# Kernel optimization log

Hardware: AMD Instinct MI355X
Metric: run time of the kernel (lower is better)

## Reference

```python
import jax, jax.numpy as jnp
import numpy as np

LUT_DIM = 33  # standard 33^3 color LUT


def setup_inputs() -> dict:
    key = jax.random.key(0)
    k1, k2 = jax.random.split(key)
    # learned 3D LUT: [out_channels=3, D_b, D_g, D_r]
    lut = jax.random.normal(k1, (3, LUT_DIM, LUT_DIM, LUT_DIM), dtype=jnp.float32) * 0.1
    # input image batch in [0, 1): [B, 3, H, W]
    x = jax.random.uniform(k2, (4, 3, 1024, 1024), dtype=jnp.float32)
    return {"lut": lut, "x": x}


def reference(lut, x):
    """Trilinear interpolation of a 3D color LUT (image-adaptive-3DLUT forward).

    lut: [3, D, D, D] laid out as lut[c, ib, ig, ir] (flat index ir + ig*D + ib*D*D)
    x:   [B, 3, H, W] with channels (r, g, b) in [0, 1]
    returns: [B, 3, H, W]
    """
    dim = lut.shape[-1]
    scale = dim - 1  # 1 / binsize

    r, g, b = x[:, 0], x[:, 1], x[:, 2]  # each [B, H, W]

    def cell(c):
        s = c * scale
        idx = jnp.clip(jnp.floor(s), 0, scale - 1).astype(jnp.int32)
        return idx, s - idx.astype(s.dtype)  # integer cell, fractional offset

    ir, dr = cell(r)
    ig, dg = cell(g)
    ib, db = cell(b)

    lut_flat = lut.reshape(3, -1)  # [3, D^3], tiny and cache-resident

    out = jnp.zeros((3,) + r.shape, dtype=x.dtype)  # [3, B, H, W]
    # 8 corners of the enclosing LUT cell, trilinear weights
    for or_ in (0, 1):
        wr = dr if or_ else (1.0 - dr)
        for og in (0, 1):
            wg = dg if og else (1.0 - dg)
            for ob in (0, 1):
                wb = db if ob else (1.0 - db)
                flat = ((ib + ob) * dim + (ig + og)) * dim + (ir + or_)  # [B, H, W]
                corner = lut_flat[:, flat]  # gather -> [3, B, H, W]
                out = out + (wr * wg * wb)[None] * corner

    return jnp.transpose(out, (1, 0, 2, 3))  # [B, 3, H, W]
```

## Files before the change

### kernel.cpp

```cpp
#include <hip/hip_runtime.h>
#include <hip/hip_fp16.h>


#define LUT_D     33
#define LUT_DD    (LUT_D * LUT_D)
#define LUT_N     (LUT_D * LUT_D * LUT_D)
#define CH_STRIDE 35940
#define STAGE_G   (CH_STRIDE / 4)
#define HW4       (1024 * 1024 / 4)
#define NGROUPS   (4 * HW4)
#define NCHUNKS   256
#define THREADS   1024
#define ITERS     (NGROUPS / NCHUNKS / THREADS)

typedef float vfloat4 __attribute__((ext_vector_type(4)));

__device__ __forceinline__ unsigned int pack2(float a, float b) {
    union { __half2 h; unsigned int u; } cv;
    cv.h = __floats2half2_rn(a, b);
    return cv.u;
}
__device__ __forceinline__ float2 unpack2(unsigned int p) {
    union { unsigned int u; __half2 h; } cv;
    cv.u = p;
    return __half22float2(cv.h);
}

__global__ __launch_bounds__(256)
void lut_pack_kernel(const float* __restrict__ lut, unsigned int* __restrict__ W) {
    const int t = blockIdx.x * 256 + (int)threadIdx.x;
    if (t >= 3 * LUT_N) return;
    const int c = t / LUT_N;
    const int i = t - c * LUT_N;
    const float a = lut[t];
    const float b = (i + 1 < LUT_N) ? lut[t + 1] : 0.0f;
    W[c * CH_STRIDE + i] = pack2(a, b);
}

__global__ __launch_bounds__(THREADS)
void lut3d_trilerp_kernel(const unsigned int* __restrict__ W,
                          const float* __restrict__ x,
                          float* __restrict__ out) {
    extern __shared__ __align__(16) unsigned int P[];

    const int bx   = blockIdx.x;
    const int xcd  = bx & 7;
    const int c    = (bx >> 3) % 3;
    const int chunk = (bx / 24) * 8 + xcd;

    const unsigned int* src = W + c * CH_STRIDE;
    for (int s = 0; s < 9; ++s) {
        const int gid = s * THREADS + (int)threadIdx.x;
        if (gid < STAGE_G) {
            __builtin_amdgcn_global_load_lds(
                (const __attribute__((address_space(1))) void*)(src + gid * 4),
                (__attribute__((address_space(3))) void*)(P + gid * 4),
                16, 0, 0);
        }
    }
    __syncthreads();

    const float4* x4 = (const float4*)x;
    float4*       o4 = (float4*)out;

    const int g0 = chunk * (NGROUPS / NCHUNKS) + (int)threadIdx.x;

    float4 R[ITERS], G[ITERS], B[ITERS];
    int obase[ITERS];
#pragma unroll
    for (int it = 0; it < ITERS; ++it) {
        const int g     = g0 + it * THREADS;
        const int b_img = g >> 18;
        const int hw4   = g & (HW4 - 1);
        const int ibase = b_img * 3 * HW4 + hw4;
        R[it] = x4[ibase];
        G[it] = x4[ibase + HW4];
        B[it] = x4[ibase + 2 * HW4];
        obase[it] = ibase + c * HW4;
    }

#pragma unroll
    for (int it = 0; it < ITERS; ++it) {
        const float rr[4] = {R[it].x, R[it].y, R[it].z, R[it].w};
        const float gg[4] = {G[it].x, G[it].y, G[it].z, G[it].w};
        const float bb[4] = {B[it].x, B[it].y, B[it].z, B[it].w};

        int   idx[4];
        float dr[4], dg[4], db[4];
#pragma unroll
        for (int k = 0; k < 4; ++k) {
            const float sr = rr[k] * 32.0f;
            const float sg = gg[k] * 32.0f;
            const float sb = bb[k] * 32.0f;
            const float fr = fminf(fmaxf(floorf(sr), 0.0f), 31.0f);
            const float fg = fminf(fmaxf(floorf(sg), 0.0f), 31.0f);
            const float fb = fminf(fmaxf(floorf(sb), 0.0f), 31.0f);
            dr[k] = sr - fr;
            dg[k] = sg - fg;
            db[k] = sb - fb;
            idx[k] = ((int)fb * LUT_D + (int)fg) * LUT_D + (int)fr;
        }

        unsigned int q00[4], q01[4], q10[4], q11[4];
#pragma unroll
        for (int k = 0; k < 4; ++k) {
            q00[k] = P[idx[k]];
            q01[k] = P[idx[k] + LUT_D];
            q10[k] = P[idx[k] + LUT_DD];
            q11[k] = P[idx[k] + LUT_DD + LUT_D];
        }

        float oo[4];
#pragma unroll
        for (int k = 0; k < 4; ++k) {
            const float2 a00 = unpack2(q00[k]);
            const float2 a01 = unpack2(q01[k]);
            const float2 a10 = unpack2(q10[k]);
            const float2 a11 = unpack2(q11[k]);
            const float l00 = a00.x + dr[k] * (a00.y - a00.x);
            const float l01 = a01.x + dr[k] * (a01.y - a01.x);
            const float l10 = a10.x + dr[k] * (a10.y - a10.x);
            const float l11 = a11.x + dr[k] * (a11.y - a11.x);
            const float l0  = l00 + dg[k] * (l01 - l00);
            const float l1  = l10 + dg[k] * (l11 - l10);
            oo[k] = l0 + db[k] * (l1 - l0);
        }

        vfloat4 v = {oo[0], oo[1], oo[2], oo[3]};
        __builtin_nontemporal_store(v, (vfloat4*)&o4[obase[it]]);
    }
}

extern "C" void kernel_launch(void* const* d_in, const int* in_sizes, int n_in,
                              void* d_out, int out_size, void* d_ws, size_t ws_size,
                              hipStream_t stream) {
    const float*  lut = (const float*)d_in[0];
    const float*  x   = (const float*)d_in[1];
    float*        out = (float*)d_out;
    unsigned int* W   = (unsigned int*)d_ws;

    const int pack_grid = (3 * LUT_N + 255) / 256;
    lut_pack_kernel<<<pack_grid, 256, 0, stream>>>(lut, W);

    const int grid = 3 * NCHUNKS;
    const size_t lds_bytes = (size_t)STAGE_G * 16;
    lut3d_trilerp_kernel<<<grid, THREADS, lds_bytes, stream>>>(W, x, out);
}
```

Baseline: 118.0 us.

## Store LUT as plain fp16 in LDS, halving footprint, and double grid chunks

Replaces the paired half2 LUT layout (each entry plus its r-neighbour) with a plain fp16 array, halving LDS per block to about 72KB. Each pixel now does 8 scalar half LDS reads instead of 4 packed 32-bit reads. Chunk count doubles to 512, input loads are interleaved with compute instead of prefetched, and the launch bound requests higher occupancy. The aim is more resident blocks per CU to hide latency, at the cost of twice as many LDS gather instructions and more staging overhead from the larger grid.

```diff
diff --git a/kernel.cpp b/kernel.cpp
--- a/kernel.cpp
+++ b/kernel.cpp
@@ -2,59 +2,47 @@
 #include <hip/hip_fp16.h>
 
 
-#define LUT_D     33
-#define LUT_DD    (LUT_D * LUT_D)
-#define LUT_N     (LUT_D * LUT_D * LUT_D)
-#define CH_STRIDE 35940
-#define STAGE_G   (CH_STRIDE / 4)
-#define HW4       (1024 * 1024 / 4)
-#define NGROUPS   (4 * HW4)
-#define NCHUNKS   256
-#define THREADS   1024
-#define ITERS     (NGROUPS / NCHUNKS / THREADS)
+#define LUT_D    33
+#define LUT_DD   (LUT_D * LUT_D)
+#define LUT_N    (LUT_D * LUT_D * LUT_D)
+#define CH_H     36000
+#define STAGE_G4 4500
+#define HW4      (1024 * 1024 / 4)
+#define NG       (4 * HW4)
+#define NCHUNKS  512
+#define THREADS  1024
+#define GPB      (NG / NCHUNKS)
+#define ITERS    (GPB / THREADS)
 
 typedef float vfloat4 __attribute__((ext_vector_type(4)));
 
-__device__ __forceinline__ unsigned int pack2(float a, float b) {
-    union { __half2 h; unsigned int u; } cv;
-    cv.h = __floats2half2_rn(a, b);
-    return cv.u;
-}
-__device__ __forceinline__ float2 unpack2(unsigned int p) {
-    union { unsigned int u; __half2 h; } cv;
-    cv.u = p;
-    return __half22float2(cv.h);
-}
-
 __global__ __launch_bounds__(256)
-void lut_pack_kernel(const float* __restrict__ lut, unsigned int* __restrict__ W) {
+void lut_pack_kernel(const float* __restrict__ lut, __half* __restrict__ W) {
     const int t = blockIdx.x * 256 + (int)threadIdx.x;
     if (t >= 3 * LUT_N) return;
     const int c = t / LUT_N;
     const int i = t - c * LUT_N;
-    const float a = lut[t];
-    const float b = (i + 1 < LUT_N) ? lut[t + 1] : 0.0f;
-    W[c * CH_STRIDE + i] = pack2(a, b);
+    W[c * CH_H + i] = __float2half(lut[t]);
 }
 
-__global__ __launch_bounds__(THREADS)
-void lut3d_trilerp_kernel(const unsigned int* __restrict__ W,
+__global__ __launch_bounds__(THREADS, 8)
+void lut3d_trilerp_kernel(const __half* __restrict__ W,
                           const float* __restrict__ x,
                           float* __restrict__ out) {
-    extern __shared__ __align__(16) unsigned int P[];
+    extern __shared__ __align__(16) __half sl[];
 
-    const int bx   = blockIdx.x;
-    const int xcd  = bx & 7;
-    const int c    = (bx >> 3) % 3;
+    const int bx    = blockIdx.x;
+    const int xcd   = bx & 7;
+    const int c     = (bx >> 3) % 3;
     const int chunk = (bx / 24) * 8 + xcd;
 
-    const unsigned int* src = W + c * CH_STRIDE;
-    for (int s = 0; s < 9; ++s) {
+    const char* srcb = (const char*)W + (size_t)c * (CH_H * 2);
+    for (int s = 0; s < 5; ++s) {
         const int gid = s * THREADS + (int)threadIdx.x;
-        if (gid < STAGE_G) {
+        if (gid < STAGE_G4) {
             __builtin_amdgcn_global_load_lds(
-                (const __attribute__((address_space(1))) void*)(src + gid * 4),
-                (__attribute__((address_space(3))) void*)(P + gid * 4),
+                (const __attribute__((address_space(1))) void*)(srcb + gid * 16),
+                (__attribute__((address_space(3))) void*)((char*)sl + gid * 16),
                 16, 0, 0);
         }
     }
@@ -63,35 +51,30 @@
     const float4* x4 = (const float4*)x;
     float4*       o4 = (float4*)out;
 
-    const int g0 = chunk * (NGROUPS / NCHUNKS) + (int)threadIdx.x;
+    const int g0 = chunk * GPB + (int)threadIdx.x;
 
-    float4 R[ITERS], G[ITERS], B[ITERS];
-    int obase[ITERS];
 #pragma unroll
     for (int it = 0; it < ITERS; ++it) {
         const int g     = g0 + it * THREADS;
         const int b_img = g >> 18;
         const int hw4   = g & (HW4 - 1);
         const int ibase = b_img * 3 * HW4 + hw4;
-        R[it] = x4[ibase];
-        G[it] = x4[ibase + HW4];
-        B[it] = x4[ibase + 2 * HW4];
-        obase[it] = ibase + c * HW4;
-    }
 
-#pragma unroll
-    for (int it = 0; it < ITERS; ++it) {
-        const float rr[4] = {R[it].x, R[it].y, R[it].z, R[it].w};
-        const float gg[4] = {G[it].x, G[it].y, G[it].z, G[it].w};
-        const float bb[4] = {B[it].x, B[it].y, B[it].z, B[it].w};
+        const float4 r4 = x4[ibase];
+        const float4 g4 = x4[ibase + HW4];
+        const float4 b4 = x4[ibase + 2 * HW4];
+
+        const float RR[4] = {r4.x, r4.y, r4.z, r4.w};
+        const float GG[4] = {g4.x, g4.y, g4.z, g4.w};
+        const float BB[4] = {b4.x, b4.y, b4.z, b4.w};
 
         int   idx[4];
         float dr[4], dg[4], db[4];
 #pragma unroll
         for (int k = 0; k < 4; ++k) {
-            const float sr = rr[k] * 32.0f;
-            const float sg = gg[k] * 32.0f;
-            const float sb = bb[k] * 32.0f;
+            const float sr = RR[k] * 32.0f;
+            const float sg = GG[k] * 32.0f;
+            const float sb = BB[k] * 32.0f;
             const float fr = fminf(fmaxf(floorf(sr), 0.0f), 31.0f);
             const float fg = fminf(fmaxf(floorf(sg), 0.0f), 31.0f);
             const float fb = fminf(fmaxf(floorf(sb), 0.0f), 31.0f);
@@ -101,48 +84,60 @@
             idx[k] = ((int)fb * LUT_D + (int)fg) * LUT_D + (int)fr;
         }
 
-        unsigned int q00[4], q01[4], q10[4], q11[4];
-#pragma unroll
-        for (int k = 0; k < 4; ++k) {
-            q00[k] = P[idx[k]];
-            q01[k] = P[idx[k] + LUT_D];
-            q10[k] = P[idx[k] + LUT_DD];
-            q11[k] = P[idx[k] + LUT_DD + LUT_D];
-        }
-
         float oo[4];
 #pragma unroll
-        for (int k = 0; k < 4; ++k) {
-            const float2 a00 = unpack2(q00[k]);
-            const float2 a01 = unpack2(q01[k]);
-            const float2 a10 = unpack2(q10[k]);
-            const float2 a11 = unpack2(q11[k]);
-            const float l00 = a00.x + dr[k] * (a00.y - a00.x);
-            const float l01 = a01.x + dr[k] * (a01.y - a01.x);
-            const float l10 = a10.x + dr[k] * (a10.y - a10.x);
-            const float l11 = a11.x + dr[k] * (a11.y - a11.x);
-            const float l0  = l00 + dg[k] * (l01 - l00);
-            const float l1  = l10 + dg[k] * (l11 - l10);
-            oo[k] = l0 + db[k] * (l1 - l0);
+        for (int kk = 0; kk < 4; kk += 2) {
+            __half h[2][8];
+#pragma unroll
+            for (int j = 0; j < 2; ++j) {
+                const int i0 = idx[kk + j];
+                h[j][0] = sl[i0];
+                h[j][1] = sl[i0 + 1];
+                h[j][2] = sl[i0 + LUT_D];
+                h[j][3] = sl[i0 + LUT_D + 1];
+                h[j][4] = sl[i0 + LUT_DD];
+                h[j][5] = sl[i0 + LUT_DD + 1];
+                h[j][6] = sl[i0 + LUT_DD + LUT_D];
+                h[j][7] = sl[i0 + LUT_DD + LUT_D + 1];
+            }
+#pragma unroll
+            for (int j = 0; j < 2; ++j) {
+                const int k = kk + j;
+                const float v000 = __half2float(h[j][0]);
+                const float v001 = __half2float(h[j][1]);
+                const float v010 = __half2float(h[j][2]);
+                const float v011 = __half2float(h[j][3]);
+                const float v100 = __half2float(h[j][4]);
+                const float v101 = __half2float(h[j][5]);
+                const float v110 = __half2float(h[j][6]);
+                const float v111 = __half2float(h[j][7]);
+                const float l00 = v000 + dr[k] * (v001 - v000);
+                const float l01 = v010 + dr[k] * (v011 - v010);
+                const float l10 = v100 + dr[k] * (v101 - v100);
+                const float l11 = v110 + dr[k] * (v111 - v110);
+                const float l0  = l00 + dg[k] * (l01 - l00);
+                const float l1  = l10 + dg[k] * (l11 - l10);
+                oo[k] = l0 + db[k] * (l1 - l0);
+            }
         }
 
         vfloat4 v = {oo[0], oo[1], oo[2], oo[3]};
-        __builtin_nontemporal_store(v, (vfloat4*)&o4[obase[it]]);
+        __builtin_nontemporal_store(v, (vfloat4*)&o4[ibase + c * HW4]);
     }
 }
 
 extern "C" void kernel_launch(void* const* d_in, const int* in_sizes, int n_in,
                               void* d_out, int out_size, void* d_ws, size_t ws_size,
                               hipStream_t stream) {
-    const float*  lut = (const float*)d_in[0];
-    const float*  x   = (const float*)d_in[1];
-    float*        out = (float*)d_out;
-    unsigned int* W   = (unsigned int*)d_ws;
+    const float* lut = (const float*)d_in[0];
+    const float* x   = (const float*)d_in[1];
+    float*       out = (float*)d_out;
+    __half*      W   = (__half*)d_ws;
 
     const int pack_grid = (3 * LUT_N + 255) / 256;
     lut_pack_kernel<<<pack_grid, 256, 0, stream>>>(lut, W);
 
     const int grid = 3 * NCHUNKS;
-    const size_t lds_bytes = (size_t)STAGE_G * 16;
+    const size_t lds_bytes = (size_t)CH_H * 2;
     lut3d_trilerp_kernel<<<grid, THREADS, lds_bytes, stream>>>(W, x, out);
 }
```

Result: slower. 171.9 us (+45.7%).

## Software-pipeline pixel loads and LDS gathers with double buffering

Applied to the files above, without the earlier changes.

Replaces the load-everything-then-compute loop with a two-stage software pipeline. Input loads run two iterations ahead and index computation plus LDS gathers run one iteration ahead of the interpolation math and store. The first input loads are now issued before the LUT-staging barrier, so they overlap with the LDS fill. This targets exposed global-memory and LDS latency and lowers register pressure from holding all iterations' inputs at once, but the fully unrolled macro code may still leave the compiler's schedule largely unchanged.

```diff
diff --git a/kernel.cpp b/kernel.cpp
--- a/kernel.cpp
+++ b/kernel.cpp
@@ -8,10 +8,10 @@
 #define CH_STRIDE 35940
 #define STAGE_G   (CH_STRIDE / 4)
 #define HW4       (1024 * 1024 / 4)
-#define NGROUPS   (4 * HW4)
+#define NG        (4 * HW4)
 #define NCHUNKS   256
 #define THREADS   1024
-#define ITERS     (NGROUPS / NCHUNKS / THREADS)
+#define ITERS     (NG / NCHUNKS / THREADS)
 
 typedef float vfloat4 __attribute__((ext_vector_type(4)));
 
@@ -20,7 +20,7 @@
     cv.h = __floats2half2_rn(a, b);
     return cv.u;
 }
-__device__ __forceinline__ float2 unpack2(unsigned int p) {
+__device__ __forceinline__ float2 up2(unsigned int p) {
     union { unsigned int u; __half2 h; } cv;
     cv.u = p;
     return __half22float2(cv.h);
@@ -43,9 +43,9 @@
                           float* __restrict__ out) {
     extern __shared__ __align__(16) unsigned int P[];
 
-    const int bx   = blockIdx.x;
-    const int xcd  = bx & 7;
-    const int c    = (bx >> 3) % 3;
+    const int bx    = blockIdx.x;
+    const int xcd   = bx & 7;
+    const int c     = (bx >> 3) % 3;
     const int chunk = (bx / 24) * 8 + xcd;
 
     const unsigned int* src = W + c * CH_STRIDE;
@@ -58,77 +58,108 @@
                 16, 0, 0);
         }
     }
-    __syncthreads();
 
     const float4* x4 = (const float4*)x;
     float4*       o4 = (float4*)out;
+    const int g0 = chunk * (NG / NCHUNKS) + (int)threadIdx.x;
 
-    const int g0 = chunk * (NGROUPS / NCHUNKS) + (int)threadIdx.x;
+    float4 Rx[2], Gx[2], Bx[2];
+    int    obase_t[ITERS];
+    int    idxA[2][4];
+    float  drA[2][4], dgA[2][4], dbA[2][4];
+    unsigned int q[2][4][4];
 
-    float4 R[ITERS], G[ITERS], B[ITERS];
-    int obase[ITERS];
-#pragma unroll
-    for (int it = 0; it < ITERS; ++it) {
-        const int g     = g0 + it * THREADS;
-        const int b_img = g >> 18;
-        const int hw4   = g & (HW4 - 1);
-        const int ibase = b_img * 3 * HW4 + hw4;
-        R[it] = x4[ibase];
-        G[it] = x4[ibase + HW4];
-        B[it] = x4[ibase + 2 * HW4];
-        obase[it] = ibase + c * HW4;
+#define LOAD_X(t, buf)                                              \
+    {                                                               \
+        const int g     = g0 + (t) * THREADS;                       \
+        const int b_img = g >> 18;                                  \
+        const int hw4   = g & (HW4 - 1);                            \
+        const int ibase = b_img * 3 * HW4 + hw4;                    \
+        Rx[buf] = x4[ibase];                                        \
+        Gx[buf] = x4[ibase + HW4];                                  \
+        Bx[buf] = x4[ibase + 2 * HW4];                              \
+        obase_t[t] = ibase + c * HW4;                               \
     }
 
+#define COMP_IDX(buf)                                               \
+    {                                                               \
+        const float RR[4] = {Rx[buf].x, Rx[buf].y, Rx[buf].z, Rx[buf].w}; \
+        const float GG[4] = {Gx[buf].x, Gx[buf].y, Gx[buf].z, Gx[buf].w}; \
+        const float BB[4] = {Bx[buf].x, Bx[buf].y, Bx[buf].z, Bx[buf].w}; \
+        _Pragma("unroll")                                           \
+        for (int k = 0; k < 4; ++k) {                               \
+            const float sr = RR[k] * 32.0f;                         \
+            const float sg = GG[k] * 32.0f;                         \
+            const float sb = BB[k] * 32.0f;                         \
+            const float fr = fminf(fmaxf(floorf(sr), 0.0f), 31.0f); \
+            const float fg = fminf(fmaxf(floorf(sg), 0.0f), 31.0f); \
+            const float fb = fminf(fmaxf(floorf(sb), 0.0f), 31.0f); \
+            drA[buf][k] = sr - fr;                                  \
+            dgA[buf][k] = sg - fg;                                  \
+            dbA[buf][k] = sb - fb;                                  \
+            idxA[buf][k] = ((int)fb * LUT_D + (int)fg) * LUT_D + (int)fr; \
+        }                                                           \
+    }
+
+#define GATHER(buf)                                                 \
+    {                                                               \
+        _Pragma("unroll")                                           \
+        for (int k = 0; k < 4; ++k) {                               \
+            const int i0 = idxA[buf][k];                            \
+            const int i1 = i0 + LUT_DD;                             \
+            q[buf][k][0] = P[i0];                                   \
+            q[buf][k][1] = P[i0 + LUT_D];    \
+            q[buf][k][2] = P[i1];                                   \
+            q[buf][k][3] = P[i1 + LUT_D];    \
+        }                                                           \
+    }
+
+#define MATH_STORE(buf, t)                                          \
+    {                                                               \
+        float oo[4];                                                \
+        _Pragma("unroll")                                           \
+        for (int k = 0; k < 4; ++k) {                               \
+            const float2 a = up2(q[buf][k][0]);                     \
+            const float2 b = up2(q[buf][k][1]);                     \
+            const float2 e = up2(q[buf][k][2]);                     \
+            const float2 d = up2(q[buf][k][3]);                     \
+            const float dr = drA[buf][k];                           \
+            const float dg = dgA[buf][k];                           \
+            const float db = dbA[buf][k];                           \
+            const float l00 = a.x + dr * (a.y - a.x);               \
+            const float l01 = b.x + dr * (b.y - b.x);               \
+            const float l10 = e.x + dr * (e.y - e.x);               \
+            const float l11 = d.x + dr * (d.y - d.x);               \
+            const float l0  = l00 + dg * (l01 - l00);               \
+            const float l1  = l10 + dg * (l11 - l10);               \
+            oo[k] = l0 + db * (l1 - l0);                            \
+        }                                                           \
+        vfloat4 v = {oo[0], oo[1], oo[2], oo[3]};                   \
+        __builtin_nontemporal_store(v, (vfloat4*)&o4[obase_t[t]]);  \
+    }
+
+    LOAD_X(0, 0);
+    LOAD_X(1, 1);
+    __syncthreads();
+
+    COMP_IDX(0);
+    GATHER(0);
+
 #pragma unroll
-    for (int it = 0; it < ITERS; ++it) {
-        const float rr[4] = {R[it].x, R[it].y, R[it].z, R[it].w};
-        const float gg[4] = {G[it].x, G[it].y, G[it].z, G[it].w};
-        const float bb[4] = {B[it].x, B[it].y, B[it].z, B[it].w};
-
-        int   idx[4];
-        float dr[4], dg[4], db[4];
-#pragma unroll
-        for (int k = 0; k < 4; ++k) {
-            const float sr = rr[k] * 32.0f;
-            const float sg = gg[k] * 32.0f;
-            const float sb = bb[k] * 32.0f;
-            const float fr = fminf(fmaxf(floorf(sr), 0.0f), 31.0f);
-            const float fg = fminf(fmaxf(floorf(sg), 0.0f), 31.0f);
-            const float fb = fminf(fmaxf(floorf(sb), 0.0f), 31.0f);
-            dr[k] = sr - fr;
-            dg[k] = sg - fg;
-            db[k] = sb - fb;
-            idx[k] = ((int)fb * LUT_D + (int)fg) * LUT_D + (int)fr;
+    for (int t = 0; t < ITERS; ++t) {
+        const int cur = t & 1;
+        const int nxt = cur ^ 1;
+        if (t + 2 < ITERS) LOAD_X(t + 2, cur);
+        if (t + 1 < ITERS) {
+            COMP_IDX(nxt);
+            GATHER(nxt);
         }
-
-        unsigned int q00[4], q01[4], q10[4], q11[4];
-#pragma unroll
-        for (int k = 0; k < 4; ++k) {
-            q00[k] = P[idx[k]];
-            q01[k] = P[idx[k] + LUT_D];
-            q10[k] = P[idx[k] + LUT_DD];
-            q11[k] = P[idx[k] + LUT_DD + LUT_D];
-        }
-
-        float oo[4];
-#pragma unroll
-        for (int k = 0; k < 4; ++k) {
-            const float2 a00 = unpack2(q00[k]);
-            const float2 a01 = unpack2(q01[k]);
-            const float2 a10 = unpack2(q10[k]);
-            const float2 a11 = unpack2(q11[k]);
-            const float l00 = a00.x + dr[k] * (a00.y - a00.x);
-            const float l01 = a01.x + dr[k] * (a01.y - a01.x);
-            const float l10 = a10.x + dr[k] * (a10.y - a10.x);
-            const float l11 = a11.x + dr[k] * (a11.y - a11.x);
-            const float l0  = l00 + dg[k] * (l01 - l00);
-            const float l1  = l10 + dg[k] * (l11 - l10);
-            oo[k] = l0 + db[k] * (l1 - l0);
-        }
-
-        vfloat4 v = {oo[0], oo[1], oo[2], oo[3]};
-        __builtin_nontemporal_store(v, (vfloat4*)&o4[obase[it]]);
+        MATH_STORE(cur, t);
     }
+#undef LOAD_X
+#undef COMP_IDX
+#undef GATHER
+#undef MATH_STORE
 }
 
 extern "C" void kernel_launch(void* const* d_in, const int* in_sizes, int n_in,
```

After: 120.5 us. 2.1% more time.
